# Kernel tuning notes

Hardware: AMD Instinct MI355X
Metric: run time of the kernel (lower is better)

The kernel has to match this reference:

```python
import jax, jax.numpy as jnp
import numpy as np

B, T, M, HE, HD = 512, 256, 81, 256, 256


def setup_inputs() -> dict:
    key = jax.random.key(0)
    ks = iter(jax.random.split(key, 32))
    def rn(shape, s=0.05):
        return (jax.random.normal(next(ks), shape, jnp.float32) * s)
    return dict(
        x=jax.random.normal(next(ks), (B, T, M), jnp.float32),
        y_history=jax.random.normal(next(ks), (B, T - 1), jnp.float32),
        # encoder input attention: Linear(2*HE->T), Linear(T->1) (input side), Linear(T->1) (score)
        W_ah=rn((T, 2 * HE)), b_ah=rn((T,)),
        W_ai=rn((1, T)), b_ai=rn((1,)),
        W_a=rn((1, T)), b_a=rn((1,)),
        # encoder LSTM (input M -> HE), PyTorch gate order i,f,g,o
        Wih_e=rn((4 * HE, M)), Whh_e=rn((4 * HE, HE)), bih_e=rn((4 * HE,)), bhh_e=rn((4 * HE,)),
        # decoder temporal attention: Linear(2*HD+HE -> HE), Linear(HE -> 1)
        W_d1=rn((HE, 2 * HD + HE)), b_d1=rn((HE,)),
        W_d2=rn((1, HE)), b_d2=rn((1,)),
        # decoder fc (HE+1 -> 1); original uses normal_() init
        W_fc=rn((1, HE + 1), 1.0), b_fc=rn((1,)),
        # decoder LSTM (input 1 -> HD)
        Wih_d=rn((4 * HD, 1)), Whh_d=rn((4 * HD, HD)), bih_d=rn((4 * HD,)), bhh_d=rn((4 * HD,)),
        # fc_final (HE+HD -> 1)
        W_ff=rn((1, HE + HD)), b_ff=rn((1,)),
    )


def _lstm_step(x, h, c, Wih, Whh, bih, bhh):
    # PyTorch LSTM cell: gates ordered (i, f, g, o)
    g = x @ Wih.T + bih + h @ Whh.T + bhh
    i, f, gg, o = jnp.split(g, 4, axis=-1)
    c = jax.nn.sigmoid(f) * c + jax.nn.sigmoid(i) * jnp.tanh(gg)
    h = jax.nn.sigmoid(o) * jnp.tanh(c)
    return h, c


def reference(x, y_history, W_ah, b_ah, W_ai, b_ai, W_a, b_a,
              Wih_e, Whh_e, bih_e, bhh_e,
              W_d1, b_d1, W_d2, b_d2, W_fc, b_fc,
              Wih_d, Whh_d, bih_d, bhh_d, W_ff, b_ff):
    dt = x.dtype
    # ---- Encoder: input attention + LSTM over T steps ----
    # attn_layer_input depends only on the full driver series -> precompute once: [B, M]
    attn_in = jnp.einsum('btm,t->bm', x, W_ai[0]) + b_ai[0]

    def enc_step(carry, xt):  # xt: [B, M]
        h, c = carry
        hc = jnp.concatenate([h, c], axis=-1)               # [B, 2*HE]
        hid_proj = hc @ W_ah.T + b_ah                       # [B, T]
        z = jnp.tanh(hid_proj[:, None, :] + attn_in[:, :, None])  # [B, M, T]
        score = jnp.einsum('bmt,t->bm', z, W_a[0]) + b_a[0]
        aw = jax.nn.softmax(score, axis=-1)                 # softmax over M drivers
        wi = aw * xt                                        # weighted input [B, M]
        h, c = _lstm_step(wi, h, c, Wih_e, Whh_e, bih_e, bhh_e)
        return (h, c), h

    h0 = jnp.zeros((B, HE), dt)
    (_, _), enc_t = jax.lax.scan(enc_step, (h0, h0), jnp.swapaxes(x, 0, 1))
    input_encoded = jnp.swapaxes(enc_t, 0, 1)               # [B, T, HE]

    # ---- Decoder: temporal attention + LSTM over T-1 steps ----
    W_d1_hc, W_d1_enc = W_d1[:, :2 * HD], W_d1[:, 2 * HD:]
    enc_proj = jnp.einsum('bte,he->bth', input_encoded, W_d1_enc)  # [B, T, HE]

    def dec_step(carry, yt):  # yt: [B]
        h, c = carry
        hc = jnp.concatenate([h, c], axis=-1)               # [B, 2*HD]
        z = jnp.tanh(enc_proj + (hc @ W_d1_hc.T + b_d1)[:, None, :])  # [B, T, HE]
        score = jnp.einsum('bth,h->bt', z, W_d2[0]) + b_d2[0]
        aw = jax.nn.softmax(score, axis=-1)                 # softmax over T
        ctx = jnp.einsum('bt,bte->be', aw, input_encoded)   # [B, HE]
        y_tild = jnp.concatenate([ctx, yt[:, None]], axis=-1) @ W_fc.T + b_fc  # [B, 1]
        h, c = _lstm_step(y_tild, h, c, Wih_d, Whh_d, bih_d, bhh_d)
        return (h, c), ctx

    hd0 = jnp.zeros((B, HD), dt)
    (h_fin, _), ctxs = jax.lax.scan(dec_step, (hd0, hd0), y_history.T)
    context = ctxs[-1]                                      # context from last step
    out = jnp.concatenate([h_fin, context], axis=-1) @ W_ff.T + b_ff  # [B, 1]
    return out
```

## Files before the change

### kernel.cpp

```cpp
#include <hip/hip_runtime.h>
#include <hip/hip_bf16.h>
#include <hip/hip_fp16.h>

#define BB  512
#define TT  256
#define MM  81
#define HEE 256

#define OFF_W8AH   0
#define OFF_WE8    65536
#define OFF_W8D1   238592
#define OFF_WD8G   304128
#define OFF_ATTN   436224
#define OFF_ENCW   477696
#define OFF_ENC    608768
#define OFF_EPI    34163200
#define WS_FLOATS  50940416

typedef _Float16 hh2 __attribute__((ext_vector_type(2)));

__device__ __forceinline__ float frcp(float x) { return __builtin_amdgcn_rcpf(x); }
__device__ __forceinline__ float fsig(float x) { return frcp(1.f + __expf(-x)); }
__device__ __forceinline__ float ftanh(float x) { return 1.f - 2.f * frcp(__expf(2.f * x) + 1.f); }
__device__ __forceinline__ float rrf(float x) { return frcp(__expf(2.f * x) + 1.f); }
__device__ __forceinline__ hh2 uash2(unsigned int u) { union { unsigned int u; hh2 h; } x; x.u = u; return x.h; }
__device__ __forceinline__ float fdot2f(unsigned int a, unsigned int b, float c) {
#if __has_builtin(__builtin_amdgcn_fdot2)
  return __builtin_amdgcn_fdot2(uash2(a), uash2(b), c, false);
#else
  hh2 ha = uash2(a), hb = uash2(b);
  return c + (float)ha.x * (float)hb.x + (float)ha.y * (float)hb.y;
#endif
}
__device__ __forceinline__ ushort f2h(float x) { return __half_as_ushort(__float2half(x)); }

#if __has_builtin(__builtin_amdgcn_cvt_pk_f32_fp8) && __has_builtin(__builtin_amdgcn_cvt_pk_fp8_f32)
typedef float ff2 __attribute__((ext_vector_type(2)));
__device__ __forceinline__ float2 cvt2lo(unsigned v) { ff2 r = __builtin_amdgcn_cvt_pk_f32_fp8(v, false); return make_float2(r[0], r[1]); }
__device__ __forceinline__ float2 cvt2hi(unsigned v) { ff2 r = __builtin_amdgcn_cvt_pk_f32_fp8(v, true);  return make_float2(r[0], r[1]); }
__device__ __forceinline__ unsigned pk4_fp8(unsigned a, unsigned b) {
  float2 fa = __half22float2(*(__half2*)&a);
  float2 fb = __half22float2(*(__half2*)&b);
  int r = __builtin_amdgcn_cvt_pk_fp8_f32(fa.x, fa.y, 0, false);
  r = __builtin_amdgcn_cvt_pk_fp8_f32(fb.x, fb.y, r, true);
  return (unsigned)r;
}
#else
__device__ __forceinline__ float dec1_fp8(unsigned b) {
  unsigned s = b >> 7, ef = (b >> 3) & 0xf, m = b & 7;
  float v = (ef == 0) ? (float)m * 0.001953125f
                      : (1.f + (float)m * 0.125f) * exp2f((float)((int)ef - 7));
  return s ? -v : v;
}
__device__ __forceinline__ float2 cvt2lo(unsigned v) { return make_float2(dec1_fp8(v & 0xff), dec1_fp8((v >> 8) & 0xff)); }
__device__ __forceinline__ float2 cvt2hi(unsigned v) { return make_float2(dec1_fp8((v >> 16) & 0xff), dec1_fp8((v >> 24) & 0xff)); }
__device__ __forceinline__ unsigned enc1_fp8(float x) {
  unsigned u = __float_as_uint(x); unsigned sgn = (u >> 31) << 7;
  float ax = fabsf(x);
  if (ax < 0.0009765625f) return sgn;
  if (ax >= 448.f) return sgn | 0x7e;
  if (ax < 0.015625f) { int k = (int)rintf(ax * 512.f); return (k >= 8) ? (sgn | 0x08) : (sgn | (unsigned)k); }
  int e = (int)((u >> 23) & 0xff) - 127;
  unsigned m = u & 0x7fffff;
  unsigned mr = m + 0x7ffff + ((m >> 20) & 1);
  if (mr >= 0x800000) { mr = 0; ++e; if (e > 8) return sgn | 0x7e; }
  return sgn | (unsigned)((e + 7) << 3) | (mr >> 20);
}
__device__ __forceinline__ unsigned pk4_fp8(unsigned a, unsigned b) {
  float2 fa = __half22float2(*(__half2*)&a);
  float2 fb = __half22float2(*(__half2*)&b);
  return enc1_fp8(fa.x) | (enc1_fp8(fa.y) << 8) | (enc1_fp8(fb.x) << 16) | (enc1_fp8(fb.y) << 24);
}
#endif

__global__ void k_prep(const float* __restrict__ W_ah, const float* __restrict__ Wih_e,
                       const float* __restrict__ Whh_e, const float* __restrict__ W_d1,
                       const float* __restrict__ Wih_d, const float* __restrict__ Whh_d,
                       float* __restrict__ ws) {
  int idx = blockIdx.x * 512 + threadIdx.x;
  if (idx < 16384) {
    int k8 = idx >> 8, j = idx & 255;
    const float* wr = W_ah + (size_t)j * 512 + 8 * k8;
    union { __half2 h[4]; uint4 u; } w;
    w.h[0] = __floats2half2_rn(wr[0], wr[1]);
    w.h[1] = __floats2half2_rn(wr[2], wr[3]);
    w.h[2] = __floats2half2_rn(wr[4], wr[5]);
    w.h[3] = __floats2half2_rn(wr[6], wr[7]);
    ((uint4*)(ws + OFF_W8AH))[idx] = w.u;
  }
  if (idx < 16384) {
    int k8 = idx >> 8, j = idx & 255;
    const float* wr = W_d1 + (size_t)j * 768 + 8 * k8;
    union { __half2 h[4]; uint4 u; } w;
    w.h[0] = __floats2half2_rn(wr[0], wr[1]);
    w.h[1] = __floats2half2_rn(wr[2], wr[3]);
    w.h[2] = __floats2half2_rn(wr[4], wr[5]);
    w.h[3] = __floats2half2_rn(wr[6], wr[7]);
    ((uint4*)(ws + OFF_W8D1))[idx] = w.u;
  }
  if (idx < 43264) {
    int k2 = idx >> 8, j = idx & 255;
    auto we = [&](int g, int kk) -> float {
      if (kk < 81)  return Wih_e[(g * 256 + j) * 81 + kk];
      if (kk < 337) return Whh_e[(g * 256 + j) * 256 + (kk - 81)];
      return 0.f;
    };
    int ke = 2 * k2, ko = 2 * k2 + 1;
    union { __half2 h[4]; uint4 u; } w;
    w.h[0] = __floats2half2_rn(we(0, ke), we(0, ko));
    w.h[1] = __floats2half2_rn(we(1, ke), we(1, ko));
    w.h[2] = __floats2half2_rn(we(2, ke), we(2, ko));
    w.h[3] = __floats2half2_rn(we(3, ke), we(3, ko));
    ((uint4*)(ws + OFF_WE8))[idx] = w.u;
  }
  if (idx < 32768) {
    int r = idx >> 8, j = idx & 255;
    int gate = r >> 5, k8 = r & 31;
    const float* wr = Whh_d + (size_t)(gate * 256 + j) * 256 + 8 * k8;
    union { __half2 h[4]; uint4 u; } w;
    w.h[0] = __floats2half2_rn(wr[0], wr[1]);
    w.h[1] = __floats2half2_rn(wr[2], wr[3]);
    w.h[2] = __floats2half2_rn(wr[4], wr[5]);
    w.h[3] = __floats2half2_rn(wr[6], wr[7]);
    ((uint4*)(ws + OFF_WD8G))[idx] = w.u;
  }
}

__global__ void k_attn(const float* __restrict__ x, const float* __restrict__ W_ai,
                       const float* __restrict__ b_ai, float* __restrict__ ws) {
  __shared__ float wai[256];
  const int b = blockIdx.x, tid = threadIdx.x;
  wai[tid] = W_ai[tid];
  wai[128 + tid] = W_ai[128 + tid];
  __syncthreads();
  if (tid < MM) {
    float acc = b_ai[0];
    const float* xp = x + (size_t)b * TT * MM + tid;
    #pragma unroll 8
    for (int t = 0; t < TT; ++t) acc = fmaf(xp[t * MM], wai[t], acc);
    ws[OFF_ATTN + b * MM + tid] = acc;
  }
}

__global__ __launch_bounds__(1024, 2) void k_encoder(
    const float* __restrict__ x, const float* __restrict__ b_ah,
    const float* __restrict__ W_a, const float* __restrict__ b_a,
    const float* __restrict__ bih_e, const float* __restrict__ bhh_e,
    float* __restrict__ ws) {
  __shared__ __align__(16) float aA[2048];
  __shared__ __align__(16) float4 gA[2048];
  __shared__ __align__(16) float hpb[512];
  __shared__ __align__(16) float wa2m[256];
  __shared__ __align__(16) ushort hcb[2][512];
  __shared__ __align__(16) ushort uu[2][344];
  const int tid = threadIdx.x;
  const int j = tid & 255, q = tid >> 8;
  const int b0 = blockIdx.x * 2, b1 = b0 + 1;

  if (tid < 256) wa2m[tid] = -2.f * W_a[tid];
  if (tid < 512) { hcb[0][tid] = 0; hcb[1][tid] = 0; }
  if (tid < 344) { uu[0][tid] = 0; uu[1][tid] = 0; }
  float bahr = 0.f; float4 bias4 = {0, 0, 0, 0};
  if (tid < 512) {
    bahr = b_ah[j];
    bias4.x = bih_e[j] + bhh_e[j];
    bias4.y = bih_e[256 + j] + bhh_e[256 + j];
    bias4.z = bih_e[512 + j] + bhh_e[512 + j];
    bias4.w = bih_e[768 + j] + bhh_e[768 + j];
  }
  float ai0 = 0.f, ai1 = 0.f;
  {
    int m = tid & 127;
    if (m < MM) {
      ai0 = ws[OFF_ATTN + b0 * MM + m];
      ai1 = ws[OFF_ATTN + b1 * MM + m];
    }
  }
  const float bav = b_a[0];
  float xc0 = 0.f, xc1 = 0.f;
  if (tid < 128) {
    int bb = (tid >= 64) ? b1 : b0;
    int lane = tid & 63;
    xc0 = x[((size_t)bb * TT) * MM + lane];
    xc1 = (lane < 17) ? x[((size_t)bb * TT) * MM + 64 + lane] : 0.f;
  }
  const uint4* __restrict__ W8A = (const uint4*)(ws + OFF_W8AH);
  const uint4* __restrict__ We8 = (const uint4*)(ws + OFF_WE8);
  const uint4* __restrict__ hcq0 = (const uint4*)hcb[0];
  const uint4* __restrict__ hcq1 = (const uint4*)hcb[1];
  const unsigned int* __restrict__ u0p = (const unsigned int*)uu[0];
  const unsigned int* __restrict__ u1p = (const unsigned int*)uu[1];
  float creg = 0.f;
  __syncthreads();
  float bavw = bav;
  if (tid < 128) {
    float s = 0.f;
    #pragma unroll
    for (int i = 0; i < 64; ++i) {
      float4 v = *(const float4*)&wa2m[4 * i];
      s += v.x + v.y + v.z + v.w;
    }
    bavw = bav - 0.5f * s;
  }

  for (int t = 0; t < TT; ++t) {
    {
      float a0 = 0.f, a0b = 0.f, a1 = 0.f, a1b = 0.f;
      const int k8b = q * 16;
      #pragma unroll 4
      for (int i = 0; i < 16; ++i) {
        int k8 = k8b + i;
        uint4 wu = W8A[k8 * 256 + j];
        uint4 h0 = hcq0[k8], h1 = hcq1[k8];
        a0  = fdot2f(wu.x, h0.x, a0);  a0b = fdot2f(wu.y, h0.y, a0b);
        a0  = fdot2f(wu.z, h0.z, a0);  a0b = fdot2f(wu.w, h0.w, a0b);
        a1  = fdot2f(wu.x, h1.x, a1);  a1b = fdot2f(wu.y, h1.y, a1b);
        a1  = fdot2f(wu.z, h1.z, a1);  a1b = fdot2f(wu.w, h1.w, a1b);
      }
      aA[(q * 256 + j) * 2 + 0] = a0 + a0b;
      aA[(q * 256 + j) * 2 + 1] = a1 + a1b;
      float4 g0 = {0, 0, 0, 0}, g1 = {0, 0, 0, 0};
      const int ku0 = 41 + q * 32;
      #pragma unroll 4
      for (int i = 0; i < 32; ++i) {
        int ku = ku0 + i;
        uint4 wu = We8[ku * 256 + j];
        unsigned int ua = u0p[ku], ub = u1p[ku];
        g0.x = fdot2f(wu.x, ua, g0.x); g0.y = fdot2f(wu.y, ua, g0.y);
        g0.z = fdot2f(wu.z, ua, g0.z); g0.w = fdot2f(wu.w, ua, g0.w);
        g1.x = fdot2f(wu.x, ub, g1.x); g1.y = fdot2f(wu.y, ub, g1.y);
        g1.z = fdot2f(wu.z, ub, g1.z); g1.w = fdot2f(wu.w, ub, g1.w);
      }
      gA[(q * 2 + 0) * 256 + j] = g0;
      gA[(q * 2 + 1) * 256 + j] = g1;
    }
    __syncthreads();
    if (tid < 512) {
      int b = tid >> 8, h = tid & 255;
      hpb[2 * h + b] = aA[(0 * 256 + h) * 2 + b] + aA[(1 * 256 + h) * 2 + b] +
                       aA[(2 * 256 + h) * 2 + b] + aA[(3 * 256 + h) * 2 + b] + bahr;
    }
    __syncthreads();
    {
      int m = tid & 127, tq = tid >> 7;
      if (m < MM) {
        float e0a = 0.f, e0b = 0.f, e1a = 0.f, e1b = 0.f;
        #pragma unroll 4
        for (int i = tq * 16; i < tq * 16 + 16; ++i) {
          float4 hv = *(const float4*)&hpb[i * 4];
          float2 wv = *(const float2*)&wa2m[i * 2];
          e0a = fmaf(wv.x, rrf(hv.x + ai0), e0a);
          e0b = fmaf(wv.y, rrf(hv.z + ai0), e0b);
          e1a = fmaf(wv.x, rrf(hv.y + ai1), e1a);
          e1b = fmaf(wv.y, rrf(hv.w + ai1), e1b);
        }
        aA[(tq * 2 + 0) * 96 + m] = e0a + e0b;
        aA[(tq * 2 + 1) * 96 + m] = e1a + e1b;
      }
    }
    __syncthreads();
    if (tid < 128) {
      int wv_id = tid >> 6, lane = tid & 63;
      float v0 = bavw, v1 = bavw;
      #pragma unroll
      for (int tq = 0; tq < 8; ++tq) {
        v0 += aA[(tq * 2 + wv_id) * 96 + lane];
        if (lane < 17) v1 += aA[(tq * 2 + wv_id) * 96 + 64 + lane];
      }
      float e0 = __expf(v0);
      float e1 = (lane < 17) ? __expf(v1) : 0.f;
      float sm = e0 + e1;
      #pragma unroll
      for (int d = 1; d < 64; d <<= 1) sm += __shfl_xor(sm, d);
      float inv = frcp(sm);
      uu[wv_id][lane] = f2h(e0 * inv * xc0);
      if (lane < 17) uu[wv_id][64 + lane] = f2h(e1 * inv * xc1);
      if (t < 255) {
        int bb = wv_id ? b1 : b0;
        xc0 = x[((size_t)bb * TT + t + 1) * MM + lane];
        xc1 = (lane < 17) ? x[((size_t)bb * TT + t + 1) * MM + 64 + lane] : 0.f;
      }
    }
    __syncthreads();
    {
      const int kA = (q == 0) ? 0 : (q == 1) ? 11 : (q == 2) ? 21 : 31;
      const int kB = (q == 0) ? 11 : (q == 1) ? 21 : (q == 2) ? 31 : 41;
      float4 g0 = gA[(q * 2 + 0) * 256 + j];
      float4 g1 = gA[(q * 2 + 1) * 256 + j];
      for (int ku = kA; ku < kB; ++ku) {
        uint4 wu = We8[ku * 256 + j];
        unsigned int ua = u0p[ku], ub = u1p[ku];
        g0.x = fdot2f(wu.x, ua, g0.x); g0.y = fdot2f(wu.y, ua, g0.y);
        g0.z = fdot2f(wu.z, ua, g0.z); g0.w = fdot2f(wu.w, ua, g0.w);
        g1.x = fdot2f(wu.x, ub, g1.x); g1.y = fdot2f(wu.y, ub, g1.y);
        g1.z = fdot2f(wu.z, ub, g1.z); g1.w = fdot2f(wu.w, ub, g1.w);
      }
      gA[(q * 2 + 0) * 256 + j] = g0;
      gA[(q * 2 + 1) * 256 + j] = g1;
    }
    __syncthreads();
    if (tid < 512) {
      int b = tid >> 8, jj = tid & 255;
      float4 s0 = gA[(0 * 2 + b) * 256 + jj];
      float4 s1 = gA[(1 * 2 + b) * 256 + jj];
      float4 s2 = gA[(2 * 2 + b) * 256 + jj];
      float4 s3 = gA[(3 * 2 + b) * 256 + jj];
      float gi = s0.x + s1.x + s2.x + s3.x + bias4.x;
      float gf = s0.y + s1.y + s2.y + s3.y + bias4.y;
      float gg = s0.z + s1.z + s2.z + s3.z + bias4.z;
      float go = s0.w + s1.w + s2.w + s3.w + bias4.w;
      float c = fsig(gf) * creg + fsig(gi) * ftanh(gg);
      float h = fsig(go) * ftanh(c);
      creg = c;
      hcb[b][jj] = f2h(h);
      hcb[b][256 + jj] = f2h(c);
      uu[b][81 + jj] = f2h(h);
      ws[OFF_ENC + (((size_t)(b ? b1 : b0) * TT + t) * HEE + jj)] = h;
    }
    __syncthreads();
  }
}

__global__ __launch_bounds__(256) void k_encw(const float* __restrict__ W_fc, float* __restrict__ ws) {
  const float* __restrict__ enc = ws + OFF_ENC;
  const int wv = threadIdx.x >> 6, lane = threadIdx.x & 63;
  float4 wfc = reinterpret_cast<const float4*>(W_fc)[lane];
  for (int r = blockIdx.x * 4 + wv; r < BB * TT; r += 4096) {
    float4 e = reinterpret_cast<const float4*>(enc + (size_t)r * HEE)[lane];
    float d = e.x * wfc.x + e.y * wfc.y + e.z * wfc.z + e.w * wfc.w;
    #pragma unroll
    for (int dd = 1; dd < 64; dd <<= 1) d += __shfl_xor(d, dd);
    if (lane == 0) ws[OFF_ENCW + r] = d;
  }
}

__global__ __launch_bounds__(256) void k_encproj(const float* __restrict__ W_d1, float* __restrict__ ws) {
  __shared__ __align__(16) float le[16][256];
  const int tid = threadIdx.x;
  const int b = blockIdx.x >> 4;
  const int t0 = (blockIdx.x & 15) * 16;
  const float* __restrict__ enc = ws + OFF_ENC;
  __half* __restrict__ epH = (__half*)(ws + OFF_EPI);
  #pragma unroll
  for (int rr = 0; rr < 16; ++rr)
    le[rr][tid] = enc[((size_t)b * TT + (t0 + rr)) * HEE + tid];
  __syncthreads();
  const float4* wrow = (const float4*)(W_d1 + (size_t)tid * 768 + 512);
  float acc[16];
  #pragma unroll
  for (int r = 0; r < 16; ++r) acc[r] = 0.f;
  for (int e4 = 0; e4 < 64; ++e4) {
    float4 w = wrow[e4];
    #pragma unroll
    for (int r = 0; r < 16; ++r) {
      float4 ev = *(const float4*)&le[r][e4 * 4];
      acc[r] += ev.x * w.x + ev.y * w.y + ev.z * w.z + ev.w * w.w;
    }
  }
  #pragma unroll
  for (int rr = 0; rr < 16; ++rr)
    epH[((size_t)b * TT + (t0 + rr)) * HEE + tid] = __float2half(acc[rr]);
}

__global__ __launch_bounds__(1024, 8) void k_decoder(
    const float* __restrict__ y_history, const float* __restrict__ b_d1,
    const float* __restrict__ W_d2, const float* __restrict__ b_d2,
    const float* __restrict__ W_fc, const float* __restrict__ b_fc,
    const float* __restrict__ Wih_d,
    const float* __restrict__ bih_d, const float* __restrict__ bhh_d,
    const float* __restrict__ W_ff, const float* __restrict__ b_ff,
    float* __restrict__ ws, float* __restrict__ out) {
  __shared__ __align__(16) unsigned char ep8L[65536];
  __shared__ __align__(16) float aA[1024];
  __shared__ __align__(16) float gL[1024];
  __shared__ __align__(16) float ddp[256];
  __shared__ __align__(16) ushort hc[512];
  __shared__ __align__(16) float w2m[256];
  __shared__ __align__(16) float ybuf[256];
  __shared__ float red[2][4];
  const int tid = threadIdx.x;
  const int tp = tid & 255, q = tid >> 8;
  const int lane = tid & 63, wvid = tid >> 6;
  const int b = blockIdx.x;
  const float wfcy = W_fc[256], bfc = b_fc[0], bd2v = b_d2[0], bffv = b_ff[0];

  if (tid < 256) w2m[tid] = -2.f * W_d2[tid];
  if (tid < 512) hc[tid] = 0;
  if (tid < 255) ybuf[tid] = y_history[(size_t)b * 255 + tid] * wfcy + bfc;
  const float bd1r = b_d1[tp];
  float4 biasd, wy;
  biasd.x = bih_d[tp] + bhh_d[tp];
  biasd.y = bih_d[256 + tp] + bhh_d[256 + tp];
  biasd.z = bih_d[512 + tp] + bhh_d[512 + tp];
  biasd.w = bih_d[768 + tp] + bhh_d[768 + tp];
  wy.x = Wih_d[tp]; wy.y = Wih_d[256 + tp]; wy.z = Wih_d[512 + tp]; wy.w = Wih_d[768 + tp];
  const float wffh = W_ff[tp], wffc = W_ff[256 + tp];
  const float ewr = ws[OFF_ENCW + (size_t)b * 256 + tp];

  const uint4* __restrict__ W8 = (const uint4*)(ws + OFF_W8D1);
  const uint4* __restrict__ WG = (const uint4*)(ws + OFF_WD8G);
  const uint4* __restrict__ epg = (const uint4*)(ws + OFF_EPI);
  const uint4* __restrict__ ep16 = (const uint4*)ep8L;
  const uint4* __restrict__ hc4 = (const uint4*)hc;

  {
    #pragma unroll
    for (int k = 0; k < 4; ++k) {
      int g = k * 1024 + tid;
      int t = g >> 4, c = g & 15;
      const uint4* src = epg + (size_t)b * 8192 + t * 32 + c * 2;
      uint4 lo = src[0], hi = src[1];
      uint4 o;
      o.x = pk4_fp8(lo.x, lo.y);
      o.y = pk4_fp8(lo.z, lo.w);
      o.z = pk4_fp8(hi.x, hi.y);
      o.w = pk4_fp8(hi.z, hi.w);
      ((uint4*)ep8L)[(g & ~15) | (c ^ (t & 15))] = o;
    }
  }
  const uint4* __restrict__ epXg = epg + (size_t)b * 8192 + tp * 32 + q * 8;
  __syncthreads();
  float bd2w = bd2v;
  if (tid < 256) {
    float s = 0.f;
    #pragma unroll
    for (int i = 0; i < 64; ++i) {
      float4 v = *(const float4*)&w2m[4 * i];
      s += v.x + v.y + v.z + v.w;
    }
    bd2w = bd2v - 0.5f * s;
  }

  float hreg = 0.f, creg = 0.f;
  float escls = 0.f, invls = 0.f, esc = 0.f;

  for (int s = 0; s < 255; ++s) {
    {
      float a0 = 0.f, a1 = 0.f, a2 = 0.f, a3 = 0.f;
      const int k8b = q * 16;
      #pragma unroll 4
      for (int i = 0; i < 16; ++i) {
        int k8 = k8b + i;
        uint4 wu = W8[k8 * 256 + tp];
        uint4 hv = hc4[k8];
        a0 = fdot2f(wu.x, hv.x, a0); a1 = fdot2f(wu.y, hv.y, a1);
        a2 = fdot2f(wu.z, hv.z, a2); a3 = fdot2f(wu.w, hv.w, a3);
      }
      aA[q * 256 + tp] = (a0 + a1) + (a2 + a3);
      float g0 = 0.f, g1 = 0.f, g2 = 0.f, g3 = 0.f;
      const uint4* wg = WG + (q * 32) * 256 + tp;
      #pragma unroll 4
      for (int i = 0; i < 32; ++i) {
        uint4 wu = wg[i * 256];
        uint4 hv = hc4[i];
        g0 = fdot2f(wu.x, hv.x, g0); g1 = fdot2f(wu.y, hv.y, g1);
        g2 = fdot2f(wu.z, hv.z, g2); g3 = fdot2f(wu.w, hv.w, g3);
      }
      gL[q * 256 + tp] = (g0 + g1) + (g2 + g3);
    }
    __syncthreads();
    if (tid < 256)
      ddp[tid] = aA[tid] + aA[256 + tid] + aA[512 + tid] + aA[768 + tid] + bd1r;
    __syncthreads();
    if (s != 254) {
      float q0 = 0.f, q1 = 0.f;
      const int base = tp * 16, sw = tp & 15;
      #pragma unroll
      for (int k = 0; k < 4; ++k) {
        uint4 eu = ep16[base + ((q * 4 + k) ^ sw)];
        const int hb = q * 64 + k * 16;
        const unsigned* ed = (const unsigned*)&eu;
        #pragma unroll
        for (int dd = 0; dd < 4; ++dd) {
          const int h4 = hb + dd * 4;
          float2 xa = cvt2lo(ed[dd]), xb = cvt2hi(ed[dd]);
          float4 wf = *(const float4*)&w2m[h4];
          float4 dv = *(const float4*)&ddp[h4];
          q0 = fmaf(wf.x, rrf(xa.x + dv.x), q0);
          q1 = fmaf(wf.y, rrf(xa.y + dv.y), q1);
          q0 = fmaf(wf.z, rrf(xb.x + dv.z), q0);
          q1 = fmaf(wf.w, rrf(xb.y + dv.w), q1);
        }
      }
      aA[q * 256 + tp] = q0 + q1;
    } else {
      float q0 = 0.f, q1 = 0.f;
      #pragma unroll
      for (int k = 0; k < 8; ++k) {
        uint4 eu = epXg[k];
        const int h8 = q * 64 + k * 8;
        const __half2* eh = (const __half2*)&eu;
        #pragma unroll
        for (int jj = 0; jj < 4; ++jj) {
          float2 ea = __half22float2(eh[jj]);
          float2 wf = *(const float2*)&w2m[h8 + 2 * jj];
          float2 dv = *(const float2*)&ddp[h8 + 2 * jj];
          q0 = fmaf(wf.x, rrf(ea.x + dv.x), q0);
          q1 = fmaf(wf.y, rrf(ea.y + dv.y), q1);
        }
      }
      aA[q * 256 + tp] = q0 + q1;
    }
    __syncthreads();
    if (tid < 256) {
      float v = aA[tp] + aA[256 + tp] + aA[512 + tp] + aA[768 + tp] + bd2w;
      esc = __expf(v);
      float den = esc, num = esc * ewr;
      #pragma unroll
      for (int d = 1; d < 64; d <<= 1) { den += __shfl_xor(den, d); num += __shfl_xor(num, d); }
      if (lane == 0) { red[0][wvid] = den; red[1][wvid] = num; }
    }
    __syncthreads();
    if (tid < 256) {
      float den = red[0][0] + red[0][1] + red[0][2] + red[0][3];
      float num = red[1][0] + red[1][1] + red[1][2] + red[1][3];
      float inv = frcp(den);
      float y = num * inv + ybuf[s];
      if (s == 254) { escls = esc; invls = inv; }
      float gi = gL[tp]       + wy.x * y + biasd.x;
      float gf = gL[256 + tp] + wy.y * y + biasd.y;
      float gg = gL[512 + tp] + wy.z * y + biasd.z;
      float go = gL[768 + tp] + wy.w * y + biasd.w;
      float c = fsig(gf) * creg + fsig(gi) * ftanh(gg);
      float h = fsig(go) * ftanh(c);
      creg = c; hreg = h;
      hc[tp] = f2h(h);
      hc[256 + tp] = f2h(c);
    }
    __syncthreads();
  }

  if (tid < 256) ddp[tp] = escls * invls;
  __syncthreads();
  {
    float c0 = 0.f;
    const float* __restrict__ e32 = ws + OFF_ENC + (size_t)b * TT * HEE;
    for (int t = q * 64; t < q * 64 + 64; ++t)
      c0 = fmaf(ddp[t], e32[(size_t)t * HEE + tp], c0);
    __syncthreads();
    aA[q * 256 + tp] = c0;
  }
  __syncthreads();
  if (tid < 256) {
    float ctx = aA[tp] + aA[256 + tp] + aA[512 + tp] + aA[768 + tp];
    float p = hreg * wffh + ctx * wffc;
    #pragma unroll
    for (int d = 1; d < 64; d <<= 1) p += __shfl_xor(p, d);
    if (lane == 0) red[0][wvid] = p;
  }
  __syncthreads();
  if (tid == 0) out[b] = red[0][0] + red[0][1] + red[0][2] + red[0][3] + bffv;
}

extern "C" void kernel_launch(void* const* d_in, const int* in_sizes, int n_in,
                              void* d_out, int out_size, void* d_ws, size_t ws_size,
                              hipStream_t stream) {
  if (ws_size < (size_t)WS_FLOATS * sizeof(float)) return;
  const float* x     = (const float*)d_in[0];
  const float* y_h   = (const float*)d_in[1];
  const float* W_ah  = (const float*)d_in[2];
  const float* b_ah  = (const float*)d_in[3];
  const float* W_ai  = (const float*)d_in[4];
  const float* b_ai  = (const float*)d_in[5];
  const float* W_a   = (const float*)d_in[6];
  const float* b_a   = (const float*)d_in[7];
  const float* Wih_e = (const float*)d_in[8];
  const float* Whh_e = (const float*)d_in[9];
  const float* bih_e = (const float*)d_in[10];
  const float* bhh_e = (const float*)d_in[11];
  const float* W_d1  = (const float*)d_in[12];
  const float* b_d1  = (const float*)d_in[13];
  const float* W_d2  = (const float*)d_in[14];
  const float* b_d2  = (const float*)d_in[15];
  const float* W_fc  = (const float*)d_in[16];
  const float* b_fc  = (const float*)d_in[17];
  const float* Wih_d = (const float*)d_in[18];
  const float* Whh_d = (const float*)d_in[19];
  const float* bih_d = (const float*)d_in[20];
  const float* bhh_d = (const float*)d_in[21];
  const float* W_ff  = (const float*)d_in[22];
  const float* b_ff  = (const float*)d_in[23];
  float* ws  = (float*)d_ws;
  float* out = (float*)d_out;

  k_prep<<<256, 512, 0, stream>>>(W_ah, Wih_e, Whh_e, W_d1, Wih_d, Whh_d, ws);
  k_attn<<<512, 128, 0, stream>>>(x, W_ai, b_ai, ws);
  k_encoder<<<256, 1024, 0, stream>>>(x, b_ah, W_a, b_a, bih_e, bhh_e, ws);
  k_encw<<<1024, 256, 0, stream>>>(W_fc, ws);
  k_encproj<<<8192, 256, 0, stream>>>(W_d1, ws);
  k_decoder<<<512, 1024, 0, stream>>>(y_h, b_d1, W_d2, b_d2, W_fc, b_fc,
                                      Wih_d, bih_d, bhh_d, W_ff, b_ff, ws, out);
}
```

Before: 9.144 ms.

## Process one batch per encoder block with gate-major weight layout

The encoder kernel now handles one batch row per block instead of two and launches 512 blocks. The encoder LSTM weights are repacked gate-major with 8-wide fp16 chunks, so each quarter of the block computes one full gate using uint4 dot products against the h/c and input vectors. This shortens the per-thread work on each serial time step and cuts shared-memory reductions. In exchange, each weight load now serves one batch instead of two, so weight traffic through the caches doubles. The workspace is relaid out so the attention buffer shares space with the later encw buffer.

```diff
diff --git a/kernel.cpp b/kernel.cpp
--- a/kernel.cpp
+++ b/kernel.cpp
@@ -8,14 +8,14 @@
 #define HEE 256
 
 #define OFF_W8AH   0
-#define OFF_WE8    65536
-#define OFF_W8D1   238592
-#define OFF_WD8G   304128
-#define OFF_ATTN   436224
-#define OFF_ENCW   477696
-#define OFF_ENC    608768
-#define OFF_EPI    34163200
-#define WS_FLOATS  50940416
+#define OFF_WEG    65536
+#define OFF_W8D1   241664
+#define OFF_WD8G   307200
+#define OFF_ENCW   438272
+#define OFF_ATTN   438272
+#define OFF_ENC    569344
+#define OFF_EPI    34123776
+#define WS_FLOATS  50900992
 
 typedef _Float16 hh2 __attribute__((ext_vector_type(2)));
 
@@ -98,20 +98,29 @@
     w.h[3] = __floats2half2_rn(wr[6], wr[7]);
     ((uint4*)(ws + OFF_W8D1))[idx] = w.u;
   }
-  if (idx < 43264) {
-    int k2 = idx >> 8, j = idx & 255;
-    auto we = [&](int g, int kk) -> float {
-      if (kk < 81)  return Wih_e[(g * 256 + j) * 81 + kk];
-      if (kk < 337) return Whh_e[(g * 256 + j) * 256 + (kk - 81)];
-      return 0.f;
-    };
-    int ke = 2 * k2, ko = 2 * k2 + 1;
+  if (idx < 44032) {
+    int gate = idx / 11008;
+    int rem = idx - gate * 11008;
+    int k8 = rem >> 8, j = rem & 255;
+    float v[8];
+    #pragma unroll
+    for (int l = 0; l < 8; ++l) {
+      float w = 0.f;
+      if (k8 < 11) {
+        int ui = 8 * k8 + l;
+        if (ui < 81) w = Wih_e[(size_t)(gate * 256 + j) * 81 + ui];
+      } else {
+        int hi = 8 * (k8 - 11) + l;
+        w = Whh_e[(size_t)(gate * 256 + j) * 256 + hi];
+      }
+      v[l] = w;
+    }
     union { __half2 h[4]; uint4 u; } w;
-    w.h[0] = __floats2half2_rn(we(0, ke), we(0, ko));
-    w.h[1] = __floats2half2_rn(we(1, ke), we(1, ko));
-    w.h[2] = __floats2half2_rn(we(2, ke), we(2, ko));
-    w.h[3] = __floats2half2_rn(we(3, ke), we(3, ko));
-    ((uint4*)(ws + OFF_WE8))[idx] = w.u;
+    w.h[0] = __floats2half2_rn(v[0], v[1]);
+    w.h[1] = __floats2half2_rn(v[2], v[3]);
+    w.h[2] = __floats2half2_rn(v[4], v[5]);
+    w.h[3] = __floats2half2_rn(v[6], v[7]);
+    ((uint4*)(ws + OFF_WEG))[idx] = w.u;
   }
   if (idx < 32768) {
     int r = idx >> 8, j = idx & 255;
@@ -142,58 +151,49 @@
   }
 }
 
-__global__ __launch_bounds__(1024, 2) void k_encoder(
+__global__ __launch_bounds__(1024, 8) void k_encoder(
     const float* __restrict__ x, const float* __restrict__ b_ah,
     const float* __restrict__ W_a, const float* __restrict__ b_a,
     const float* __restrict__ bih_e, const float* __restrict__ bhh_e,
     float* __restrict__ ws) {
-  __shared__ __align__(16) float aA[2048];
-  __shared__ __align__(16) float4 gA[2048];
-  __shared__ __align__(16) float hpb[512];
+  __shared__ __align__(16) float aA[1024];
+  __shared__ __align__(16) float gL[1024];
+  __shared__ __align__(16) float hp[256];
   __shared__ __align__(16) float wa2m[256];
-  __shared__ __align__(16) ushort hcb[2][512];
-  __shared__ __align__(16) ushort uu[2][344];
+  __shared__ __align__(16) ushort hc[512];
+  __shared__ __align__(16) ushort upad[352];
   const int tid = threadIdx.x;
-  const int j = tid & 255, q = tid >> 8;
-  const int b0 = blockIdx.x * 2, b1 = b0 + 1;
+  const int tp = tid & 255, q = tid >> 8;
+  const int lane = tid & 63;
+  const int b = blockIdx.x;
 
   if (tid < 256) wa2m[tid] = -2.f * W_a[tid];
-  if (tid < 512) { hcb[0][tid] = 0; hcb[1][tid] = 0; }
-  if (tid < 344) { uu[0][tid] = 0; uu[1][tid] = 0; }
+  if (tid < 512) hc[tid] = 0;
+  if (tid < 352) upad[tid] = 0;
   float bahr = 0.f; float4 bias4 = {0, 0, 0, 0};
-  if (tid < 512) {
-    bahr = b_ah[j];
-    bias4.x = bih_e[j] + bhh_e[j];
-    bias4.y = bih_e[256 + j] + bhh_e[256 + j];
-    bias4.z = bih_e[512 + j] + bhh_e[512 + j];
-    bias4.w = bih_e[768 + j] + bhh_e[768 + j];
-  }
-  float ai0 = 0.f, ai1 = 0.f;
-  {
-    int m = tid & 127;
-    if (m < MM) {
-      ai0 = ws[OFF_ATTN + b0 * MM + m];
-      ai1 = ws[OFF_ATTN + b1 * MM + m];
-    }
-  }
+  if (tid < 256) {
+    bahr = b_ah[tp];
+    bias4.x = bih_e[tp] + bhh_e[tp];
+    bias4.y = bih_e[256 + tp] + bhh_e[256 + tp];
+    bias4.z = bih_e[512 + tp] + bhh_e[512 + tp];
+    bias4.w = bih_e[768 + tp] + bhh_e[768 + tp];
+  }
+  float ai = 0.f;
+  { int m = tid & 127; if (m < MM) ai = ws[OFF_ATTN + b * MM + m]; }
   const float bav = b_a[0];
   float xc0 = 0.f, xc1 = 0.f;
-  if (tid < 128) {
-    int bb = (tid >= 64) ? b1 : b0;
-    int lane = tid & 63;
-    xc0 = x[((size_t)bb * TT) * MM + lane];
-    xc1 = (lane < 17) ? x[((size_t)bb * TT) * MM + 64 + lane] : 0.f;
+  if (tid < 64) {
+    xc0 = x[(size_t)b * TT * MM + tid];
+    xc1 = (tid < 17) ? x[(size_t)b * TT * MM + 64 + tid] : 0.f;
   }
   const uint4* __restrict__ W8A = (const uint4*)(ws + OFF_W8AH);
-  const uint4* __restrict__ We8 = (const uint4*)(ws + OFF_WE8);
-  const uint4* __restrict__ hcq0 = (const uint4*)hcb[0];
-  const uint4* __restrict__ hcq1 = (const uint4*)hcb[1];
-  const unsigned int* __restrict__ u0p = (const unsigned int*)uu[0];
-  const unsigned int* __restrict__ u1p = (const unsigned int*)uu[1];
+  const uint4* __restrict__ WEG = (const uint4*)(ws + OFF_WEG);
+  const uint4* __restrict__ hc4 = (const uint4*)hc;
+  const uint4* __restrict__ up4 = (const uint4*)upad;
   float creg = 0.f;
   __syncthreads();
   float bavw = bav;
-  if (tid < 128) {
+  if (tid < 64) {
     float s = 0.f;
     #pragma unroll
     for (int i = 0; i < 64; ++i) {
@@ -205,67 +205,56 @@
 
   for (int t = 0; t < TT; ++t) {
     {
-      float a0 = 0.f, a0b = 0.f, a1 = 0.f, a1b = 0.f;
+      float a0 = 0.f, a1 = 0.f, a2 = 0.f, a3 = 0.f;
       const int k8b = q * 16;
       #pragma unroll 4
       for (int i = 0; i < 16; ++i) {
         int k8 = k8b + i;
-        uint4 wu = W8A[k8 * 256 + j];
-        uint4 h0 = hcq0[k8], h1 = hcq1[k8];
-        a0  = fdot2f(wu.x, h0.x, a0);  a0b = fdot2f(wu.y, h0.y, a0b);
-        a0  = fdot2f(wu.z, h0.z, a0);  a0b = fdot2f(wu.w, h0.w, a0b);
-        a1  = fdot2f(wu.x, h1.x, a1);  a1b = fdot2f(wu.y, h1.y, a1b);
-        a1  = fdot2f(wu.z, h1.z, a1);  a1b = fdot2f(wu.w, h1.w, a1b);
-      }
-      aA[(q * 256 + j) * 2 + 0] = a0 + a0b;
-      aA[(q * 256 + j) * 2 + 1] = a1 + a1b;
-      float4 g0 = {0, 0, 0, 0}, g1 = {0, 0, 0, 0};
-      const int ku0 = 41 + q * 32;
+        uint4 wu = W8A[k8 * 256 + tp];
+        uint4 hv = hc4[k8];
+        a0 = fdot2f(wu.x, hv.x, a0); a1 = fdot2f(wu.y, hv.y, a1);
+        a2 = fdot2f(wu.z, hv.z, a2); a3 = fdot2f(wu.w, hv.w, a3);
+      }
+      aA[q * 256 + tp] = (a0 + a1) + (a2 + a3);
+      float g0 = 0.f, g1 = 0.f, g2 = 0.f, g3 = 0.f;
+      const uint4* wg = WEG + (q * 43 + 11) * 256 + tp;
       #pragma unroll 4
       for (int i = 0; i < 32; ++i) {
-        int ku = ku0 + i;
-        uint4 wu = We8[ku * 256 + j];
-        unsigned int ua = u0p[ku], ub = u1p[ku];
-        g0.x = fdot2f(wu.x, ua, g0.x); g0.y = fdot2f(wu.y, ua, g0.y);
-        g0.z = fdot2f(wu.z, ua, g0.z); g0.w = fdot2f(wu.w, ua, g0.w);
-        g1.x = fdot2f(wu.x, ub, g1.x); g1.y = fdot2f(wu.y, ub, g1.y);
-        g1.z = fdot2f(wu.z, ub, g1.z); g1.w = fdot2f(wu.w, ub, g1.w);
-      }
-      gA[(q * 2 + 0) * 256 + j] = g0;
-      gA[(q * 2 + 1) * 256 + j] = g1;
-    }
-    __syncthreads();
-    if (tid < 512) {
-      int b = tid >> 8, h = tid & 255;
-      hpb[2 * h + b] = aA[(0 * 256 + h) * 2 + b] + aA[(1 * 256 + h) * 2 + b] +
-                       aA[(2 * 256 + h) * 2 + b] + aA[(3 * 256 + h) * 2 + b] + bahr;
-    }
+        uint4 wu = wg[i * 256];
+        uint4 hv = hc4[i];
+        g0 = fdot2f(wu.x, hv.x, g0); g1 = fdot2f(wu.y, hv.y, g1);
+        g2 = fdot2f(wu.z, hv.z, g2); g3 = fdot2f(wu.w, hv.w, g3);
+      }
+      gL[q * 256 + tp] = (g0 + g1) + (g2 + g3);
+    }
+    __syncthreads();
+    if (tid < 256)
+      hp[tp] = aA[tp] + aA[256 + tp] + aA[512 + tp] + aA[768 + tp] + bahr;
     __syncthreads();
     {
       int m = tid & 127, tq = tid >> 7;
       if (m < MM) {
-        float e0a = 0.f, e0b = 0.f, e1a = 0.f, e1b = 0.f;
-        #pragma unroll 4
-        for (int i = tq * 16; i < tq * 16 + 16; ++i) {
-          float4 hv = *(const float4*)&hpb[i * 4];
-          float2 wv = *(const float2*)&wa2m[i * 2];
-          e0a = fmaf(wv.x, rrf(hv.x + ai0), e0a);
-          e0b = fmaf(wv.y, rrf(hv.z + ai0), e0b);
-          e1a = fmaf(wv.x, rrf(hv.y + ai1), e1a);
-          e1b = fmaf(wv.y, rrf(hv.w + ai1), e1b);
+        float e0a = 0.f, e0b = 0.f;
+        const int i0 = tq * 8;
+        #pragma unroll
+        for (int it = 0; it < 8; ++it) {
+          float4 hv = *(const float4*)&hp[(i0 + it) * 4];
+          float4 wv = *(const float4*)&wa2m[(i0 + it) * 4];
+          e0a = fmaf(wv.x, rrf(hv.x + ai), e0a);
+          e0b = fmaf(wv.y, rrf(hv.y + ai), e0b);
+          e0a = fmaf(wv.z, rrf(hv.z + ai), e0a);
+          e0b = fmaf(wv.w, rrf(hv.w + ai), e0b);
         }
-        aA[(tq * 2 + 0) * 96 + m] = e0a + e0b;
-        aA[(tq * 2 + 1) * 96 + m] = e1a + e1b;
-      }
-    }
-    __syncthreads();
-    if (tid < 128) {
-      int wv_id = tid >> 6, lane = tid & 63;
+        aA[tq * 128 + m] = e0a + e0b;
+      }
+    }
+    __syncthreads();
+    if (tid < 64) {
       float v0 = bavw, v1 = bavw;
       #pragma unroll
       for (int tq = 0; tq < 8; ++tq) {
-        v0 += aA[(tq * 2 + wv_id) * 96 + lane];
-        if (lane < 17) v1 += aA[(tq * 2 + wv_id) * 96 + 64 + lane];
+        v0 += aA[tq * 128 + lane];
+        if (lane < 17) v1 += aA[tq * 128 + 64 + lane];
       }
       float e0 = __expf(v0);
       float e1 = (lane < 17) ? __expf(v1) : 0.f;
@@ -273,49 +262,39 @@
       #pragma unroll
       for (int d = 1; d < 64; d <<= 1) sm += __shfl_xor(sm, d);
       float inv = frcp(sm);
-      uu[wv_id][lane] = f2h(e0 * inv * xc0);
-      if (lane < 17) uu[wv_id][64 + lane] = f2h(e1 * inv * xc1);
+      upad[lane] = f2h(e0 * inv * xc0);
+      if (lane < 17) upad[64 + lane] = f2h(e1 * inv * xc1);
       if (t < 255) {
-        int bb = wv_id ? b1 : b0;
-        xc0 = x[((size_t)bb * TT + t + 1) * MM + lane];
-        xc1 = (lane < 17) ? x[((size_t)bb * TT + t + 1) * MM + 64 + lane] : 0.f;
+        xc0 = x[((size_t)b * TT + t + 1) * MM + lane];
+        xc1 = (lane < 17) ? x[((size_t)b * TT + t + 1) * MM + 64 + lane] : 0.f;
       }
     }
     __syncthreads();
     {
-      const int kA = (q == 0) ? 0 : (q == 1) ? 11 : (q == 2) ? 21 : 31;
-      const int kB = (q == 0) ? 11 : (q == 1) ? 21 : (q == 2) ? 31 : 41;
-      float4 g0 = gA[(q * 2 + 0) * 256 + j];
-      float4 g1 = gA[(q * 2 + 1) * 256 + j];
-      for (int ku = kA; ku < kB; ++ku) {
-        uint4 wu = We8[ku * 256 + j];
-        unsigned int ua = u0p[ku], ub = u1p[ku];
-        g0.x = fdot2f(wu.x, ua, g0.x); g0.y = fdot2f(wu.y, ua, g0.y);
-        g0.z = fdot2f(wu.z, ua, g0.z); g0.w = fdot2f(wu.w, ua, g0.w);
-        g1.x = fdot2f(wu.x, ub, g1.x); g1.y = fdot2f(wu.y, ub, g1.y);
-        g1.z = fdot2f(wu.z, ub, g1.z); g1.w = fdot2f(wu.w, ub, g1.w);
-      }
-      gA[(q * 2 + 0) * 256 + j] = g0;
-      gA[(q * 2 + 1) * 256 + j] = g1;
-    }
-    __syncthreads();
-    if (tid < 512) {
-      int b = tid >> 8, jj = tid & 255;
-      float4 s0 = gA[(0 * 2 + b) * 256 + jj];
-      float4 s1 = gA[(1 * 2 + b) * 256 + jj];
-      float4 s2 = gA[(2 * 2 + b) * 256 + jj];
-      float4 s3 = gA[(3 * 2 + b) * 256 + jj];
-      float gi = s0.x + s1.x + s2.x + s3.x + bias4.x;
-      float gf = s0.y + s1.y + s2.y + s3.y + bias4.y;
-      float gg = s0.z + s1.z + s2.z + s3.z + bias4.z;
-      float go = s0.w + s1.w + s2.w + s3.w + bias4.w;
+      float g0 = 0.f, g1 = 0.f;
+      const uint4* wg = WEG + (q * 43) * 256 + tp;
+      #pragma unroll
+      for (int i = 0; i < 11; ++i) {
+        uint4 wu = wg[i * 256];
+        uint4 uv = up4[i];
+        g0 = fdot2f(wu.x, uv.x, g0); g1 = fdot2f(wu.y, uv.y, g1);
+        g0 = fdot2f(wu.z, uv.z, g0); g1 = fdot2f(wu.w, uv.w, g1);
+      }
+      gL[q * 256 + tp] += g0 + g1;
+    }
+    __syncthreads();
+    if (tid < 256) {
+      float gi = gL[tp] + bias4.x;
+      float gf = gL[256 + tp] + bias4.y;
+      float gg = gL[512 + tp] + bias4.z;
+      float go = gL[768 + tp] + bias4.w;
       float c = fsig(gf) * creg + fsig(gi) * ftanh(gg);
       float h = fsig(go) * ftanh(c);
       creg = c;
-      hcb[b][jj] = f2h(h);
-      hcb[b][256 + jj] = f2h(c);
-      uu[b][81 + jj] = f2h(h);
-      ws[OFF_ENC + (((size_t)(b ? b1 : b0) * TT + t) * HEE + jj)] = h;
+      hc[tp] = f2h(h);
+      hc[256 + tp] = f2h(c);
+      upad[88 + tp] = f2h(h);
+      ws[OFF_ENC + (((size_t)b * TT + t) * HEE + tp)] = h;
     }
     __syncthreads();
   }
@@ -585,7 +564,7 @@
 
   k_prep<<<256, 512, 0, stream>>>(W_ah, Wih_e, Whh_e, W_d1, Wih_d, Whh_d, ws);
   k_attn<<<512, 128, 0, stream>>>(x, W_ai, b_ai, ws);
-  k_encoder<<<256, 1024, 0, stream>>>(x, b_ah, W_a, b_a, bih_e, bhh_e, ws);
+  k_encoder<<<512, 1024, 0, stream>>>(x, b_ah, W_a, b_a, bih_e, bhh_e, ws);
   k_encw<<<1024, 256, 0, stream>>>(W_fc, ws);
   k_encproj<<<8192, 256, 0, stream>>>(W_d1, ws);
   k_decoder<<<512, 1024, 0, stream>>>(y_h, b_d1, W_d2, b_d2, W_fc, b_fc,
```

After: 12.26 ms. 1.34x slower.
